# Kernel tuning notes

Measured on AMD Instinct MI355X. Metric: run time of the kernel, lower is better.

Reference implementation:

```python
import jax, jax.numpy as jnp
import numpy as np

NUM_ENTITY = 500000
NUM_RELATION = 6000
NUM_WORD = 200000
D = 100          # entity_dim == word_dim
L = 3            # num_layer
B, E, F, Q = 16, 2000, 8000, 20
PAGERANK_LAMBDA = 0.8
FACT_SCALE = 3.0
VERY_NEG = -1e11
VERY_SMALL = 1e-10


def setup_inputs() -> dict:
    key = jax.random.key(0)
    ks = jax.random.split(key, 24)
    s = 0.05
    return {
        'local_entity': jax.random.randint(ks[0], (B, E), 0, NUM_ENTITY),
        'kb_fact_rel': jax.random.randint(ks[1], (B, F), 0, NUM_RELATION),
        'kb_head': jax.random.randint(ks[2], (B, F), 0, E),
        'kb_tail': jax.random.randint(ks[3], (B, F), 0, E),
        'query_text': jax.random.randint(ks[4], (B, Q), 0, NUM_WORD),
        'q2e_adj_mat': jax.random.uniform(ks[5], (B, E, 1)),
        'entity_table': jax.random.normal(ks[6], (NUM_ENTITY + 1, D)) * s,
        'rel_table': jax.random.normal(ks[7], (NUM_RELATION + 1, D)) * s,
        'word_table': jax.random.normal(ks[8], (NUM_WORD + 1, D)) * s,
        'rel_lin_w': jax.random.normal(ks[9], (D, D)) * s,
        'rel_lin_b': jnp.zeros((D,)),
        'lstm_wih': jax.random.normal(ks[10], (4 * D, D)) * s,
        'lstm_whh': jax.random.normal(ks[11], (4 * D, D)) * s,
        'lstm_bih': jnp.zeros((4 * D,)),
        'lstm_bhh': jnp.zeros((4 * D,)),
        'q2e_w': jax.random.normal(ks[12], (L, D, D)) * s,
        'q2e_b': jnp.zeros((L, D)),
        'e2q_w': jax.random.normal(ks[13], (L, D, 3 * D)) * s,
        'e2q_b': jnp.zeros((L, D)),
        'e2e_w': jax.random.normal(ks[14], (L, D, 3 * D)) * s,
        'e2e_b': jnp.zeros((L, D)),
        'head_w': jax.random.normal(ks[15], (L, D, D)) * s,
        'head_b': jnp.zeros((L, D)),
        'tail_w': jax.random.normal(ks[16], (L, D, D)) * s,
        'tail_b': jnp.zeros((L, D)),
        'self_w': jax.random.normal(ks[17], (L, D, D)) * s,
        'self_b': jnp.zeros((L, D)),
        'score_w': jax.random.normal(ks[18], (1, D)) * s,
        'score_b': jnp.zeros((1,)),
    }


def _lstm(x, wih, whh, bih, bhh):
    # x: (B, Q, D); torch LSTM gate order i,f,g,o
    b = x.shape[0]
    h0 = jnp.zeros((b, D), x.dtype)

    def step(carry, xt):
        h, c = carry
        g = xt @ wih.T + h @ whh.T + bih + bhh
        i, f, gg, o = jnp.split(g, 4, axis=-1)
        c = jax.nn.sigmoid(f) * c + jax.nn.sigmoid(i) * jnp.tanh(gg)
        h = jax.nn.sigmoid(o) * jnp.tanh(c)
        return (h, c), h

    (h, _), hs = jax.lax.scan(step, (h0, h0), x.transpose(1, 0, 2))
    return hs.transpose(1, 0, 2), h


def _gather(x, idx):
    # sparse_bmm(entity2fact, x): out[b,f] = x[b, head[b,f]]
    return jnp.take_along_axis(x, idx[:, :, None], axis=1)


def _scatter(x, idx, num):
    # sparse_bmm(fact2entity, x): segment-sum facts onto tail entities
    b, f, d = x.shape
    flat = (idx + jnp.arange(b)[:, None] * num).reshape(-1)
    return jax.ops.segment_sum(x.reshape(b * f, d), flat, num_segments=b * num).reshape(b, num, d)


def reference(local_entity, kb_fact_rel, kb_head, kb_tail, query_text, q2e_adj_mat,
              entity_table, rel_table, word_table, rel_lin_w, rel_lin_b,
              lstm_wih, lstm_whh, lstm_bih, lstm_bhh,
              q2e_w, q2e_b, e2q_w, e2q_b, e2e_w, e2e_b,
              head_w, head_b, tail_w, tail_b, self_w, self_b, score_w, score_b):
    div = float(np.sqrt(D))
    q_mask = (query_text != NUM_WORD).astype(jnp.float32)
    e_mask = (local_entity != NUM_ENTITY).astype(jnp.float32)

    # query LSTM encoding
    q_emb = word_table[query_text]                                   # (B,Q,D)
    q_hidden, q_last = _lstm(q_emb, lstm_wih, lstm_whh, lstm_bih, lstm_bhh)
    query_node_emb = q_last[:, None, :]                              # (B,1,D)

    # fact embeddings from relations
    fact_emb = rel_table[kb_fact_rel] @ rel_lin_w.T + rel_lin_b      # (B,F,D)

    # fact-to-query attention weights (softmax over query words)
    sim = jnp.einsum('bqd,bfd->bqf', q_hidden, fact_emb) / div
    sim = jax.nn.softmax(sim + (1.0 - q_mask)[:, :, None] * VERY_NEG, axis=1)
    att = jnp.einsum('bqf,bqd->bfd', sim, q_hidden)                  # (B,F,D)
    Wf = jnp.sum(att * fact_emb, axis=2) / div                       # (B,F)
    W_tilde = jnp.exp(Wf - Wf.max(axis=1, keepdims=True))
    e2f_softmax = jnp.clip(_scatter(W_tilde[:, :, None], kb_head, E)[:, :, 0], VERY_SMALL, None)

    local_entity_emb = entity_table[local_entity]                    # (B,E,D)
    pagerank_f = q2e_adj_mat[:, :, 0]                                # (B,E)

    for i in range(L):
        q2e_emb = jnp.broadcast_to(query_node_emb @ q2e_w[i].T + q2e_b[i], (B, E, D))
        # entity -> fact (gather heads)
        e2f = jax.nn.relu(fact_emb @ self_w[i].T + self_b[i] +
                          _gather(local_entity_emb @ head_w[i].T + head_b[i], kb_head))
        e2f = e2f * (W_tilde[:, :, None] * _gather((pagerank_f / e2f_softmax)[:, :, None], kb_head))
        # fact -> entity (scatter to tails)
        f2e = jax.nn.relu(local_entity_emb @ self_w[i].T + self_b[i] +
                          FACT_SCALE * _scatter(e2f @ tail_w[i].T + tail_b[i], kb_tail, E))
        # pagerank propagation
        pr = _scatter(_gather(pagerank_f[:, :, None], kb_head), kb_tail, E)[:, :, 0]
        pagerank_f = PAGERANK_LAMBDA * pr + (1.0 - PAGERANK_LAMBDA) * pagerank_f
        # k=3 concat -> e2q / e2e updates
        nxt = jnp.concatenate([local_entity_emb, q2e_emb, f2e], axis=2)   # (B,E,3D)
        query_node_emb = jnp.einsum('be,bed->bd', pagerank_f, nxt @ e2q_w[i].T + e2q_b[i])[:, None, :]
        local_entity_emb = jax.nn.relu(nxt @ e2e_w[i].T + e2e_b[i])

    score = (local_entity_emb @ score_w.T + score_b)[:, :, 0]
    return score + (1.0 - e_mask) * VERY_NEG
```

## Files before the change

### kernel.cpp

```cpp
#include <hip/hip_runtime.h>
#include <math.h>

namespace {

typedef unsigned short u16;
typedef short bf16x8 __attribute__((ext_vector_type(8)));
typedef float f32x4 __attribute__((ext_vector_type(4)));

constexpr int B = 16, E = 2000, F = 8000, Q = 20, D = 100, NLAYER = 3;
constexpr int NUM_ENTITY_C = 500000;
constexpr int NREL1 = 6001;
constexpr int SK = 128;
constexpr int WFSZ = 28 * 64 * 8;
constexpr float PAGERANK_LAMBDA = 0.8f;
constexpr float FACT_SCALE = 3.0f;
constexpr float VERY_NEG = -100000000000.0f;
constexpr float VERY_SMALL = 1e-10f;

__device__ __forceinline__ float sigf(float x) { return 1.0f / (1.0f + __expf(-x)); }

__device__ __forceinline__ short f2bf(float f) {
    union { float f; unsigned int u; } c; c.f = f;
    unsigned int u = c.u + 0x7FFF + ((c.u >> 16) & 1);
    return (short)(u >> 16);
}
__device__ __forceinline__ float bf2f(u16 s) {
    union { unsigned int u; float f; } c; c.u = ((unsigned int)s) << 16;
    return c.f;
}

__global__ void wprep_kernel(const float* __restrict__ rel_lin_w,
                             const float* __restrict__ self_w, const float* __restrict__ head_w,
                             const float* __restrict__ tail_w, const float* __restrict__ e2e_w,
                             u16* __restrict__ WF)
{
    int m = blockIdx.y;
    int ns = blockIdx.x;
    int n = ns >> 2, s = ns & 3;
    int lane = threadIdx.x;
    const float* W; int ldW = D, kofs = 0; float scale = 1.f;
    if (m == 0) { W = rel_lin_w; }
    else {
        int L = (m - 1) / 5, t = (m - 1) % 5;
        if (t == 0)      { W = self_w + (size_t)L * D * D; }
        else if (t == 1) { W = head_w + (size_t)L * D * D; }
        else if (t == 2) { W = tail_w + (size_t)L * D * D; scale = FACT_SCALE; }
        else if (t == 3) { W = e2e_w + (size_t)L * D * 3 * D; ldW = 3 * D; }
        else             { W = e2e_w + (size_t)L * D * 3 * D; ldW = 3 * D; kofs = 2 * D; }
    }
    int col = n * 16 + (lane & 15);
    int kb = s * 32 + (lane >> 4) * 8;
    bf16x8 f;
#pragma unroll
    for (int j = 0; j < 8; ++j) {
        int k = kb + j;
        float v = (col < D && k < D) ? scale * W[(size_t)col * ldW + kofs + k] : 0.f;
        f[j] = f2bf(v);
    }
    *reinterpret_cast<bf16x8*>(WF + ((size_t)m * 28 + ns) * 64 * 8 + lane * 8) = f;
}

__global__ void qhprep_kernel(const float* __restrict__ qh, u16* __restrict__ qhB)
{
    int b = blockIdx.x;
    int t = threadIdx.x;
    int ns = t >> 6;
    int lane = t & 63;
    int n = ns >> 2, s = ns & 3;
    int q = n * 16 + (lane & 15);
    int kb = s * 32 + (lane >> 4) * 8;
    bf16x8 f;
#pragma unroll
    for (int j = 0; j < 8; ++j) {
        int k = kb + j;
        float v = (q < Q && k < D) ? qh[((size_t)b * Q + q) * D + k] : 0.f;
        f[j] = f2bf(v);
    }
    *reinterpret_cast<bf16x8*>(qhB + ((size_t)(b * 8 + ns) * 64 + lane) * 8) = f;
}

__global__ __launch_bounds__(256, 2) void wfm_kernel(const u16* __restrict__ REL,
                                                     const int* __restrict__ frel,
                                                     const u16* __restrict__ qhB,
                                                     float* __restrict__ wt, int nrows)
{
    const int lane = threadIdx.x & 63;
    const int lrow = lane & 15, lkg = lane >> 4;
    const int wv = blockIdx.x * (blockDim.x >> 6) + (threadIdx.x >> 6);
    const int nwv = gridDim.x * (blockDim.x >> 6);
    const int nch = nrows >> 4;

    for (int chunk = wv; chunk < nch; chunk += nwv) {
        const int row = chunk * 16 + lrow;
        const int b = (chunk * 16) / F;
        bf16x8 af[4];
        {
            const u16* src = REL + (size_t)frel[row] * SK;
#pragma unroll
            for (int s = 0; s < 4; ++s)
                af[s] = *reinterpret_cast<const bf16x8*>(src + s * 32 + lkg * 8);
        }
        f32x4 acc[2];
        acc[0] = (f32x4){0.f, 0.f, 0.f, 0.f};
        acc[1] = (f32x4){0.f, 0.f, 0.f, 0.f};
#pragma unroll
        for (int s = 0; s < 4; ++s) {
#pragma unroll
            for (int n = 0; n < 2; ++n) {
                bf16x8 qb = *reinterpret_cast<const bf16x8*>(
                    qhB + ((size_t)(b * 8 + n * 4 + s) * 64 + lane) * 8);
                acc[n] = __builtin_amdgcn_mfma_f32_16x16x32_bf16(af[s], qb, acc[n], 0, 0, 0);
            }
        }
        const bool v1 = lrow < (Q - 16);
#pragma unroll
        for (int r = 0; r < 4; ++r) {
            float s0 = acc[0][r] * 0.1f;
            float s1 = acc[1][r] * 0.1f;
            float m = v1 ? fmaxf(s0, s1) : s0;
#pragma unroll
            for (int d = 1; d < 16; d <<= 1) m = fmaxf(m, __shfl_xor(m, d));
            float e0 = __expf(s0 - m);
            float e1 = v1 ? __expf(s1 - m) : 0.f;
            float sum = e0 + e1;
            float wsum = fmaf(e0, s0, e1 * s1);
#pragma unroll
            for (int d = 1; d < 16; d <<= 1) {
                sum += __shfl_xor(sum, d);
                wsum += __shfl_xor(wsum, d);
            }
            if (lrow == 0) wt[chunk * 16 + lkg * 4 + r] = wsum / sum;
        }
    }
}

template<int A1S, int A2S, int EPI, bool OUTBF>
__global__ __launch_bounds__(256, 2) void mm2(
    const void* __restrict__ A1p, const int* __restrict__ idx1, int lda1,
    const void* __restrict__ A2p, const int* __restrict__ idx2,
    const u16* __restrict__ WF1, const u16* __restrict__ WF2,
    const float* __restrict__ b1, const float* __restrict__ b2,
    const float* __restrict__ vq,
    const float* __restrict__ wtv, const float* __restrict__ prv,
    const int* __restrict__ row_start,
    const float* __restrict__ prOld, const int* __restrict__ sheadv,
    float* __restrict__ prNew,
    void* __restrict__ outp, int nrows)
{
    const int lane = threadIdx.x & 63;
    const int lrow = lane & 15, lkg = lane >> 4;
    const int wv = blockIdx.x * (blockDim.x >> 6) + (threadIdx.x >> 6);
    const int nwv = gridDim.x * (blockDim.x >> 6);
    const int nch = (nrows + 15) >> 4;

    bf16x8 w1[7][4];
#pragma unroll
    for (int n = 0; n < 7; ++n)
#pragma unroll
        for (int s = 0; s < 4; ++s)
            w1[n][s] = *reinterpret_cast<const bf16x8*>(WF1 + ((size_t)(n * 4 + s) * 64 + lane) * 8);

    for (int chunk = wv; chunk < nch; chunk += nwv) {
        const int row = chunk * 16 + lrow;
        const int ar = row < nrows ? row : nrows - 1;

        bf16x8 af1[4];
        if (A1S == 0) {
            const u16* src = (const u16*)A1p + (size_t)ar * SK;
#pragma unroll
            for (int s = 0; s < 4; ++s)
                af1[s] = *reinterpret_cast<const bf16x8*>(src + s * 32 + lkg * 8);
        } else if (A1S == 1) {
            const u16* src = (const u16*)A1p + (size_t)idx1[ar] * SK;
#pragma unroll
            for (int s = 0; s < 4; ++s)
                af1[s] = *reinterpret_cast<const bf16x8*>(src + s * 32 + lkg * 8);
        } else {
            const float* arow = (const float*)A1p + (size_t)ar * lda1;
#pragma unroll
            for (int s = 0; s < 4; ++s) {
                const int k0 = s * 32 + lkg * 8;
                float tv[8];
                if (k0 + 8 <= D) {
                    float4 v0 = *reinterpret_cast<const float4*>(arow + k0);
                    float4 v1 = *reinterpret_cast<const float4*>(arow + k0 + 4);
                    tv[0]=v0.x; tv[1]=v0.y; tv[2]=v0.z; tv[3]=v0.w;
                    tv[4]=v1.x; tv[5]=v1.y; tv[6]=v1.z; tv[7]=v1.w;
                } else {
#pragma unroll
                    for (int j = 0; j < 8; ++j) tv[j] = (k0 + j < D) ? arow[k0 + j] : 0.f;
                }
                bf16x8 f;
#pragma unroll
                for (int j = 0; j < 8; ++j) f[j] = f2bf(tv[j]);
                af1[s] = f;
            }
        }

        int s0 = 0, s1 = 0;
        if (A2S == 2) { s0 = row_start[ar]; s1 = row_start[ar + 1]; }

        bf16x8 af2[4];
        if (A2S == 1) {
            const u16* src = (const u16*)A2p + (size_t)idx2[ar] * SK;
#pragma unroll
            for (int s = 0; s < 4; ++s)
                af2[s] = *reinterpret_cast<const bf16x8*>(src + s * 32 + lkg * 8);
        } else if (A2S == 3) {
            const u16* src = (const u16*)A2p + (size_t)ar * SK;
#pragma unroll
            for (int s = 0; s < 4; ++s)
                af2[s] = *reinterpret_cast<const bf16x8*>(src + s * 32 + lkg * 8);
        }

        f32x4 acc[7];
#pragma unroll
        for (int n = 0; n < 7; ++n) acc[n] = (f32x4){0.f, 0.f, 0.f, 0.f};
#pragma unroll
        for (int s = 0; s < 4; ++s) {
#pragma unroll
            for (int n = 0; n < 7; ++n)
                acc[n] = __builtin_amdgcn_mfma_f32_16x16x32_bf16(af1[s], w1[n][s], acc[n], 0, 0, 0);
            if (A2S == 1 || A2S == 3) {
#pragma unroll
                for (int n = 0; n < 7; ++n) {
                    bf16x8 w2 = *reinterpret_cast<const bf16x8*>(
                        WF2 + ((size_t)(n * 4 + s) * 64 + lane) * 8);
                    acc[n] = __builtin_amdgcn_mfma_f32_16x16x32_bf16(af2[s], w2, acc[n], 0, 0, 0);
                }
            } else if (A2S == 2) {
                float a2f[8];
#pragma unroll
                for (int j = 0; j < 8; ++j) a2f[j] = 0.f;
                for (int i = s0; i < s1; ++i) {
                    bf16x8 v = *reinterpret_cast<const bf16x8*>(
                        (const u16*)A2p + (size_t)i * SK + s * 32 + lkg * 8);
#pragma unroll
                    for (int j = 0; j < 8; ++j) a2f[j] += bf2f((u16)v[j]);
                }
                bf16x8 fsum;
#pragma unroll
                for (int j = 0; j < 8; ++j) fsum[j] = f2bf(a2f[j]);
#pragma unroll
                for (int n = 0; n < 7; ++n) {
                    bf16x8 w2 = *reinterpret_cast<const bf16x8*>(
                        WF2 + ((size_t)(n * 4 + s) * 64 + lane) * 8);
                    acc[n] = __builtin_amdgcn_mfma_f32_16x16x32_bf16(fsum, w2, acc[n], 0, 0, 0);
                }
            }
        }
        if (A2S == 2 && lkg == 0 && row < nrows) {
            float a = 0.f;
            for (int i = s0; i < s1; ++i) a += prOld[sheadv[i]];
            prNew[row] = PAGERANK_LAMBDA * a + (1.0f - PAGERANK_LAMBDA) * prOld[row];
        }

        const int rb = chunk * 16 + lkg * 4;
#pragma unroll
        for (int r = 0; r < 4; ++r) {
            const int orow = rb + r;
            if (orow >= nrows) continue;
            float rsv = 1.f, cntf = 0.f; int vb = 0;
            if (EPI == 1) rsv = wtv[orow] * prv[idx2[orow]];
            if (EPI == 2) cntf = (float)(row_start[orow + 1] - row_start[orow]);
            if (EPI == 3) vb = orow / E;
#pragma unroll
            for (int n = 0; n < 7; ++n) {
                const int col = n * 16 + lrow;
                if (col >= D) continue;
                float v = acc[n][r];
                if (b1) v += b1[col];
                if (EPI == 1) v += b2[col];
                if (EPI == 2) v += FACT_SCALE * cntf * b2[col];
                if (EPI == 3) v += vq[vb * D + col];
                if (EPI != 0) v = fmaxf(v, 0.f);
                if (EPI == 1) v *= rsv;
                if (OUTBF) ((u16*)outp)[(size_t)orow * SK + col] = (u16)f2bf(v);
                else       ((float*)outp)[(size_t)orow * D + col] = v;
            }
        }
    }
}

__global__ __launch_bounds__(512) void gatesx_kernel(
    const int* __restrict__ qtext, const float* __restrict__ wtab,
    const float* __restrict__ wih, const float* __restrict__ bih,
    const float* __restrict__ bhh, float* __restrict__ gx)
{
    int row = blockIdx.x;
    int t = threadIdx.x;
    __shared__ __align__(16) float xs[D];
    if (t < D) xs[t] = wtab[(size_t)qtext[row] * D + t];
    __syncthreads();
    if (t < 4 * D) {
        const float4* w4 = reinterpret_cast<const float4*>(wih + (size_t)t * D);
        const float4* x4 = reinterpret_cast<const float4*>(xs);
        float a0 = 0.f, a1 = 0.f, a2 = 0.f, a3 = 0.f;
#pragma unroll
        for (int k = 0; k < 25; ++k) {
            float4 wv = w4[k]; float4 xv = x4[k];
            a0 = fmaf(wv.x, xv.x, a0); a1 = fmaf(wv.y, xv.y, a1);
            a2 = fmaf(wv.z, xv.z, a2); a3 = fmaf(wv.w, xv.w, a3);
        }
        gx[(size_t)row * (4 * D) + t] = a0 + a1 + a2 + a3 + bih[t] + bhh[t];
    }
}

__global__ __launch_bounds__(512) void lstmrec_kernel(
    const float* __restrict__ gx, const float* __restrict__ whh,
    float* __restrict__ q_hidden, float* __restrict__ qne)
{
    int b = blockIdx.x, t = threadIdx.x;
    __shared__ __align__(16) float h[D];
    __shared__ float cst[D];
    __shared__ float g[4 * D];
    float4 w[25];
    if (t < 4 * D) {
        const float4* wr = reinterpret_cast<const float4*>(whh + (size_t)t * D);
#pragma unroll
        for (int k = 0; k < 25; ++k) w[k] = wr[k];
    }
    if (t < D) { h[t] = 0.f; cst[t] = 0.f; }
    __syncthreads();
    for (int step = 0; step < Q; ++step) {
        if (t < 4 * D) {
            const float4* h4 = reinterpret_cast<const float4*>(h);
            float a0 = 0.f, a1 = 0.f, a2 = 0.f, a3 = 0.f;
#pragma unroll
            for (int k = 0; k < 25; ++k) {
                float4 hv = h4[k];
                a0 = fmaf(w[k].x, hv.x, a0); a1 = fmaf(w[k].y, hv.y, a1);
                a2 = fmaf(w[k].z, hv.z, a2); a3 = fmaf(w[k].w, hv.w, a3);
            }
            g[t] = a0 + a1 + a2 + a3 + gx[((size_t)b * Q + step) * (4 * D) + t];
        }
        __syncthreads();
        if (t < D) {
            float gi = g[t], gf = g[t + D], gg = g[t + 2 * D], go = g[t + 3 * D];
            float cn = sigf(gf) * cst[t] + sigf(gi) * tanhf(gg);
            float hn = sigf(go) * tanhf(cn);
            cst[t] = cn; h[t] = hn;
            q_hidden[((size_t)b * Q + step) * D + t] = hn;
            if (step == Q - 1) qne[b * D + t] = hn;
        }
        __syncthreads();
    }
}

__global__ void idxabs_kernel(const int* __restrict__ kb_head, const int* __restrict__ kb_tail,
                              int* __restrict__ headAbs, int* __restrict__ tailAbs,
                              int* __restrict__ counts)
{
    int r = blockIdx.x * 256 + threadIdx.x;
    if (r < B * F) {
        int b = r / F;
        headAbs[r] = b * E + kb_head[r];
        int t = b * E + kb_tail[r];
        tailAbs[r] = t;
        atomicAdd(&counts[t], 1);
    }
}

__global__ __launch_bounds__(1024) void scan_kernel(const int* __restrict__ counts,
                                                    int* __restrict__ row_start,
                                                    int* __restrict__ cursor)
{
    __shared__ int part[1024];
    int t = threadIdx.x;
    int base = t * 32;
    int local[32];
    int s = 0;
#pragma unroll
    for (int i = 0; i < 32; ++i) {
        int idx = base + i;
        int v = (idx < B * E) ? counts[idx] : 0;
        local[i] = s; s += v;
    }
    part[t] = s;
    __syncthreads();
    for (int off = 1; off < 1024; off <<= 1) {
        int v = (t >= off) ? part[t - off] : 0;
        __syncthreads();
        if (t >= off) part[t] += v;
        __syncthreads();
    }
    int prev = (t > 0) ? part[t - 1] : 0;
#pragma unroll
    for (int i = 0; i < 32; ++i) {
        int idx = base + i;
        if (idx < B * E) { int rs = prev + local[i]; row_start[idx] = rs; cursor[idx] = rs; }
    }
    if (t == 1023) row_start[B * E] = part[1023];
}

__global__ void fill_kernel(const int* __restrict__ tailAbs, int* __restrict__ cursor,
                            int* __restrict__ factlist)
{
    int r = blockIdx.x * 256 + threadIdx.x;
    if (r < B * F) {
        int p = atomicAdd(&cursor[tailAbs[r]], 1);
        factlist[p] = r;
    }
}

__global__ void sprep_kernel(const int* __restrict__ factlist, const int* __restrict__ frel,
                             const int* __restrict__ headAbs, const float* __restrict__ wt,
                             const float* __restrict__ e2fsm,
                             int* __restrict__ srel, int* __restrict__ shead,
                             float* __restrict__ srsv)
{
    int i = blockIdx.x * 256 + threadIdx.x;
    if (i < B * F) {
        int fl = factlist[i];
        int h = headAbs[fl];
        srel[i] = frel[fl];
        shead[i] = h;
        srsv[i] = wt[fl] / fmaxf(e2fsm[h], VERY_SMALL);
    }
}

__global__ void rowmax_kernel(const float* __restrict__ Wf, float* __restrict__ Wmax)
{
    int b = blockIdx.x, tid = threadIdx.x;
    float m = -3.4e38f;
    for (int i = tid; i < F; i += 256) m = fmaxf(m, Wf[(size_t)b * F + i]);
#pragma unroll
    for (int o = 32; o > 0; o >>= 1) m = fmaxf(m, __shfl_down(m, o));
    __shared__ float sm[4];
    if ((tid & 63) == 0) sm[tid >> 6] = m;
    __syncthreads();
    if (tid == 0) Wmax[b] = fmaxf(fmaxf(sm[0], sm[1]), fmaxf(sm[2], sm[3]));
}

__global__ void wtilde_kernel(float* __restrict__ wt, const float* __restrict__ Wmax,
                              const int* __restrict__ headAbs, float* __restrict__ e2fsm)
{
    int r = blockIdx.x * 256 + threadIdx.x;
    if (r < B * F) {
        int b = r / F;
        float v = __expf(wt[r] - Wmax[b]);
        wt[r] = v;
        atomicAdd(&e2fsm[headAbs[r]], v);
    }
}

__global__ void entgather_kernel(const int* __restrict__ local_entity,
                                 const float* __restrict__ etab, u16* __restrict__ emb,
                                 const float* __restrict__ q2e_adj, float* __restrict__ pr)
{
    int i = blockIdx.x * 256 + threadIdx.x;
    if (i < B * E) pr[i] = q2e_adj[i];
    if (i < B * E * 25) {
        int row = i / 25, p = i - row * 25;
        float4 v = reinterpret_cast<const float4*>(etab + (size_t)local_entity[row] * D)[p];
        short4 o;
        o.x = f2bf(v.x); o.y = f2bf(v.y); o.z = f2bf(v.z); o.w = f2bf(v.w);
        *reinterpret_cast<short4*>(emb + (size_t)row * SK + p * 4) = o;
    }
}

__global__ void qvec_kernel(const float* __restrict__ qne, const float* __restrict__ q2ew,
                            const float* __restrict__ q2eb, const float* __restrict__ e2ew,
                            float* __restrict__ q2e_vec, float* __restrict__ vq)
{
    int b = blockIdx.x, t = threadIdx.x;
    __shared__ float qv[D];
    __shared__ float qn[D];
    if (t < D) qn[t] = qne[b * D + t];
    __syncthreads();
    if (t < D) {
        const float* wr = q2ew + (size_t)t * D;
        float acc = q2eb[t];
        for (int k = 0; k < D; ++k) acc = fmaf(qn[k], wr[k], acc);
        qv[t] = acc; q2e_vec[b * D + t] = acc;
    }
    __syncthreads();
    if (t < D) {
        const float* wr = e2ew + (size_t)t * 300 + 100;
        float acc = 0.f;
        for (int k = 0; k < D; ++k) acc = fmaf(qv[k], wr[k], acc);
        vq[b * D + t] = acc;
    }
}

__global__ __launch_bounds__(256) void zsum_kernel(const float* __restrict__ pr,
                                                   const u16* __restrict__ emb,
                                                   const u16* __restrict__ f2e,
                                                   float* __restrict__ zpart)
{
    const int b = blockIdx.x, ch = blockIdx.y;
    const int t = threadIdx.x;
    const int g = t >> 4, tg = t & 15;
    const int ebase = ch * (E / 16);
    const int eend = ebase + (E / 16);
    float accA[8], accB[8];
#pragma unroll
    for (int j = 0; j < 8; ++j) { accA[j] = 0.f; accB[j] = 0.f; }
    float accp = 0.f;
    for (int e = ebase + g; e < eend; e += 16) {
        const float p = pr[b * E + e];
        const size_t ro = ((size_t)b * E + e) * SK + tg * 8;
        bf16x8 va = *reinterpret_cast<const bf16x8*>(emb + ro);
        bf16x8 vb = *reinterpret_cast<const bf16x8*>(f2e + ro);
#pragma unroll
        for (int j = 0; j < 8; ++j) {
            accA[j] = fmaf(p, bf2f((u16)va[j]), accA[j]);
            accB[j] = fmaf(p, bf2f((u16)vb[j]), accB[j]);
        }
        if (tg == 0) accp += p;
    }
    __shared__ float smA[16][132];
    __shared__ float smB[16][132];
    __shared__ float smp[16];
#pragma unroll
    for (int j = 0; j < 8; ++j) {
        smA[g][tg * 8 + j] = accA[j];
        smB[g][tg * 8 + j] = accB[j];
    }
    if (tg == 0) smp[g] = accp;
    __syncthreads();
    float* zp = zpart + (size_t)(b * 16 + ch) * 208;
    if (t < D) {
        float sa = 0.f, sb = 0.f;
#pragma unroll
        for (int gg = 0; gg < 16; ++gg) { sa += smA[gg][t]; sb += smB[gg][t]; }
        zp[t] = sa;
        zp[D + t] = sb;
    }
    if (t == 255) {
        float sp = 0.f;
#pragma unroll
        for (int gg = 0; gg < 16; ++gg) sp += smp[gg];
        zp[2 * D] = sp;
    }
}

__global__ void qne_kernel(const float* __restrict__ zpart, const float* __restrict__ q2ev,
                           const float* __restrict__ W, const float* __restrict__ bias,
                           float* __restrict__ qne)
{
    int b = blockIdx.x, t = threadIdx.x;
    __shared__ float zb[201];
    for (int i = t; i < 201; i += 128) {
        float s = 0.f;
        for (int ch = 0; ch < 16; ++ch) s += zpart[(size_t)(b * 16 + ch) * 208 + i];
        zb[i] = s;
    }
    __syncthreads();
    if (t >= D) return;
    float ps = zb[2 * D];
    const float* wr = W + (size_t)t * 3 * D;
    float acc = ps * bias[t];
    for (int k = 0; k < D; ++k) {
        acc = fmaf(zb[k], wr[k], acc);
        acc = fmaf(ps * q2ev[b * D + k], wr[D + k], acc);
        acc = fmaf(zb[D + k], wr[2 * D + k], acc);
    }
    qne[b * D + t] = acc;
}

__global__ __launch_bounds__(256) void score_kernel(const u16* __restrict__ emb,
                                                    const float* __restrict__ sw,
                                                    const float* __restrict__ sb,
                                                    const int* __restrict__ le,
                                                    float* __restrict__ outp)
{
    __shared__ float rows[64 * 106];
    __shared__ float sws[D];
    int r0 = blockIdx.x * 64, tid = threadIdx.x;
    for (int i = tid; i < 64 * 16; i += 256) {
        int r = i >> 4, c = i & 15;
        if (c < 13) {
            bf16x8 raw = *reinterpret_cast<const bf16x8*>(emb + (size_t)(r0 + r) * SK + c * 8);
#pragma unroll
            for (int j = 0; j < 8; ++j) rows[r * 106 + c * 8 + j] = bf2f((u16)raw[j]);
        }
    }
    if (tid < D) sws[tid] = sw[tid];
    __syncthreads();
    if (tid < 64) {
        float acc = sb[0];
        const float* rr = &rows[tid * 106];
        for (int k = 0; k < D; ++k) acc = fmaf(rr[k], sws[k], acc);
        int r = r0 + tid;
        outp[r] = acc + ((le[r] != NUM_ENTITY_C) ? 0.0f : VERY_NEG);
    }
}

int mmgrid(int nrows) {
    int ch = (nrows + 15) / 16;
    int blocks = (ch + 3) / 4;
    return blocks < 512 ? blocks : 512;
}

}

extern "C" void kernel_launch(void* const* d_in, const int* in_sizes, int n_in,
                              void* d_out, int out_size, void* d_ws, size_t ws_size,
                              hipStream_t stream)
{
    (void)in_sizes; (void)n_in; (void)out_size;
    const int*   local_entity = (const int*)d_in[0];
    const int*   kb_fact_rel  = (const int*)d_in[1];
    const int*   kb_head      = (const int*)d_in[2];
    const int*   kb_tail      = (const int*)d_in[3];
    const int*   query_text   = (const int*)d_in[4];
    const float* q2e_adj      = (const float*)d_in[5];
    const float* entity_table = (const float*)d_in[6];
    const float* rel_table    = (const float*)d_in[7];
    const float* word_table   = (const float*)d_in[8];
    const float* rel_lin_w    = (const float*)d_in[9];
    const float* rel_lin_b    = (const float*)d_in[10];
    const float* lstm_wih     = (const float*)d_in[11];
    const float* lstm_whh     = (const float*)d_in[12];
    const float* lstm_bih     = (const float*)d_in[13];
    const float* lstm_bhh     = (const float*)d_in[14];
    const float* q2e_w        = (const float*)d_in[15];
    const float* q2e_b        = (const float*)d_in[16];
    const float* e2q_w        = (const float*)d_in[17];
    const float* e2q_b        = (const float*)d_in[18];
    const float* e2e_w        = (const float*)d_in[19];
    const float* e2e_b        = (const float*)d_in[20];
    const float* head_w       = (const float*)d_in[21];
    const float* head_b       = (const float*)d_in[22];
    const float* tail_w       = (const float*)d_in[23];
    const float* tail_b       = (const float*)d_in[24];
    const float* self_w       = (const float*)d_in[25];
    const float* self_b       = (const float*)d_in[26];
    const float* score_w      = (const float*)d_in[27];
    const float* score_b      = (const float*)d_in[28];
    float* out = (float*)d_out;

    float* ws = (float*)d_ws;
    size_t o = 0;
    auto alloc = [&](size_t n) { float* p = ws + o; o += (n + 3) & ~(size_t)3; return p; };
    float* q_hidden = alloc((size_t)B * Q * D);
    float* qne      = alloc(B * D);
    float* gx       = alloc((size_t)B * Q * 4 * D);
    float* wt       = alloc((size_t)B * F);
    float* wmax     = alloc(16);
    float* e2fsm    = alloc(B * E);
    int*   counts   = (int*)alloc(B * E);
    float* pr0      = alloc(B * E);
    float* pr1      = alloc(B * E);
    float* q2e_vec  = alloc(B * D);
    float* vq       = alloc(B * D);
    float* zpart    = alloc((size_t)B * 16 * 208);
    float* srsv     = alloc((size_t)B * F);
    u16* WF   = (u16*)alloc((size_t)16 * WFSZ / 2);
    u16* qhB  = (u16*)alloc((size_t)B * 8 * 64 * 8 / 2);
    u16* REL  = (u16*)alloc((size_t)NREL1 * SK / 2 + 64);
    u16* emb0 = (u16*)alloc((size_t)B * E * SK / 2);
    u16* emb1 = (u16*)alloc((size_t)B * E * SK / 2);
    u16* e2fS = (u16*)alloc((size_t)B * F * SK / 2);
    u16* f2e  = (u16*)alloc((size_t)B * E * SK / 2);
    int* headAbs  = (int*)alloc((size_t)B * F);
    int* tailAbs  = (int*)alloc((size_t)B * F);
    int* row_start= (int*)alloc(B * E + 1);
    int* cursor   = (int*)alloc(B * E);
    int* factlist = (int*)alloc((size_t)B * F);
    int* srel     = (int*)alloc((size_t)B * F);
    int* shead    = (int*)alloc((size_t)B * F);
    if (ws_size < o * sizeof(float)) return;

    auto WFm = [&](int m) { return WF + (size_t)m * WFSZ; };

    wprep_kernel<<<dim3(28, 16), dim3(64), 0, stream>>>(rel_lin_w, self_w, head_w, tail_w,
                                                        e2e_w, WF);
    gatesx_kernel<<<dim3(B * Q), dim3(512), 0, stream>>>(query_text, word_table, lstm_wih,
                                                         lstm_bih, lstm_bhh, gx);
    lstmrec_kernel<<<dim3(B), dim3(512), 0, stream>>>(gx, lstm_whh, q_hidden, qne);
    qhprep_kernel<<<dim3(B), dim3(512), 0, stream>>>(q_hidden, qhB);
    hipMemsetAsync(e2fsm, 0, (size_t)2 * B * E * sizeof(float), stream);
    idxabs_kernel<<<dim3((B * F + 255) / 256), dim3(256), 0, stream>>>(
        kb_head, kb_tail, headAbs, tailAbs, counts);
    scan_kernel<<<dim3(1), dim3(1024), 0, stream>>>(counts, row_start, cursor);
    fill_kernel<<<dim3((B * F + 255) / 256), dim3(256), 0, stream>>>(tailAbs, cursor, factlist);

    mm2<2, 0, 0, true><<<dim3(mmgrid(NREL1)), dim3(256), 0, stream>>>(
        rel_table, nullptr, D, nullptr, nullptr, WFm(0), nullptr, rel_lin_b, nullptr,
        nullptr, nullptr, nullptr, nullptr, nullptr, nullptr, nullptr,
        REL, NREL1);

    wfm_kernel<<<dim3(mmgrid(B * F)), dim3(256), 0, stream>>>(REL, kb_fact_rel, qhB, wt, B * F);
    rowmax_kernel<<<dim3(B), dim3(256), 0, stream>>>(wt, wmax);
    wtilde_kernel<<<dim3((B * F + 255) / 256), dim3(256), 0, stream>>>(wt, wmax, headAbs, e2fsm);
    sprep_kernel<<<dim3((B * F + 255) / 256), dim3(256), 0, stream>>>(
        factlist, kb_fact_rel, headAbs, wt, e2fsm, srel, shead, srsv);
    entgather_kernel<<<dim3((B * E * 25 + 255) / 256), dim3(256), 0, stream>>>(
        local_entity, entity_table, emb0, q2e_adj, pr0);

    u16* embO = emb0; u16* embN = emb1;
    float* prO = pr0; float* prN = pr1;
    for (int i = 0; i < NLAYER; ++i) {
        const float* q2e_wi  = q2e_w + (size_t)i * D * D;
        const float* q2e_bi  = q2e_b + i * D;
        const float* e2q_wi  = e2q_w + (size_t)i * D * 3 * D;
        const float* e2q_bi  = e2q_b + i * D;
        const float* e2e_wi  = e2e_w + (size_t)i * D * 3 * D;
        const float* e2e_bi  = e2e_b + i * D;
        const float* head_bi = head_b + i * D;
        const float* tail_bi = tail_b + i * D;
        const float* self_bi = self_b + i * D;
        const u16* wf_self = WFm(1 + i * 5 + 0);
        const u16* wf_head = WFm(1 + i * 5 + 1);
        const u16* wf_tail = WFm(1 + i * 5 + 2);
        const u16* wf_e2e0 = WFm(1 + i * 5 + 3);
        const u16* wf_e2e2 = WFm(1 + i * 5 + 4);

        qvec_kernel<<<dim3(B), dim3(128), 0, stream>>>(qne, q2e_wi, q2e_bi, e2e_wi,
                                                       q2e_vec, vq);
        mm2<1, 1, 1, true><<<dim3(mmgrid(B * F)), dim3(256), 0, stream>>>(
            REL, srel, 0, embO, shead, wf_self, wf_head, self_bi, head_bi,
            nullptr, srsv, prO, nullptr, nullptr, nullptr, nullptr,
            e2fS, B * F);
        mm2<0, 2, 2, true><<<dim3(mmgrid(B * E)), dim3(256), 0, stream>>>(
            embO, nullptr, 0, e2fS, nullptr, wf_self, wf_tail, self_bi, tail_bi,
            nullptr, nullptr, nullptr, row_start, prO, shead, prN,
            f2e, B * E);
        zsum_kernel<<<dim3(B, 16), dim3(256), 0, stream>>>(prN, embO, f2e, zpart);
        qne_kernel<<<dim3(B), dim3(128), 0, stream>>>(zpart, q2e_vec, e2q_wi, e2q_bi, qne);
        mm2<0, 3, 3, true><<<dim3(mmgrid(B * E)), dim3(256), 0, stream>>>(
            embO, nullptr, 0, f2e, nullptr, wf_e2e0, wf_e2e2, e2e_bi, nullptr,
            vq, nullptr, nullptr, nullptr, nullptr, nullptr, nullptr,
            embN, B * E);
        { u16* tmp = embO; embO = embN; embN = tmp; }
        { float* tmp = prO; prO = prN; prN = tmp; }
    }
    score_kernel<<<dim3((B * E) / 64), dim3(256), 0, stream>>>(
        embO, score_w, score_b, local_entity, out);
}
```

Measured before the change: 624.3 us.

## Fuse softmax, zsum, qne, score and fact-sort steps into neighbouring kernels

Folds the exp and head-sum atomics into wfm_kernel and drops the per-batch row-max pass; the max shift cancels in the W_tilde ratio. Merges fill and sprep into one scatter kernel. Moves the pagerank-weighted z reduction into the f2e mm2 epilogue via atomics, and the e2q/qne product into the next layer's qvec kernel. Folds the score projection into the last e2e mm2 and skips pagerank/z work in the final layer. This removes several launches and a re-read of emb/f2e, at the cost of more global atomics, dropping the max shift inside exp, and a grid change for the entity-side mm2s.

Measured after the change: 738.5 us. 18.3% more time.

```diff
diff --git a/kernel.cpp b/kernel.cpp
--- a/kernel.cpp
+++ b/kernel.cpp
@@ -82,7 +82,9 @@
 __global__ __launch_bounds__(256, 2) void wfm_kernel(const u16* __restrict__ REL,
                                                      const int* __restrict__ frel,
                                                      const u16* __restrict__ qhB,
-                                                     float* __restrict__ wt, int nrows)
+                                                     const int* __restrict__ headAbs,
+                                                     float* __restrict__ wt,
+                                                     float* __restrict__ e2fsm, int nrows)
 {
     const int lane = threadIdx.x & 63;
     const int lrow = lane & 15, lkg = lane >> 4;
@@ -129,12 +131,17 @@
                 sum += __shfl_xor(sum, d);
                 wsum += __shfl_xor(wsum, d);
             }
-            if (lrow == 0) wt[chunk * 16 + lkg * 4 + r] = wsum / sum;
-        }
-    }
-}
-
-template<int A1S, int A2S, int EPI, bool OUTBF>
+            if (lrow == 0) {
+                int orow = chunk * 16 + lkg * 4 + r;
+                float wtl = __expf(wsum / sum);
+                wt[orow] = wtl;
+                atomicAdd(&e2fsm[headAbs[orow]], wtl);
+            }
+        }
+    }
+}
+
+template<int A1S, int A2S, int EPI, bool OUTBF, bool PRZ>
 __global__ __launch_bounds__(256, 2) void mm2(
     const void* __restrict__ A1p, const int* __restrict__ idx1, int lda1,
     const void* __restrict__ A2p, const int* __restrict__ idx2,
@@ -144,7 +151,7 @@
     const float* __restrict__ wtv, const float* __restrict__ prv,
     const int* __restrict__ row_start,
     const float* __restrict__ prOld, const int* __restrict__ sheadv,
-    float* __restrict__ prNew,
+    float* __restrict__ prNew, float* __restrict__ zacc,
     void* __restrict__ outp, int nrows)
 {
     const int lane = threadIdx.x & 63;
@@ -249,21 +256,34 @@
                 }
             }
         }
-        if (A2S == 2 && lkg == 0 && row < nrows) {
-            float a = 0.f;
-            for (int i = s0; i < s1; ++i) a += prOld[sheadv[i]];
-            prNew[row] = PAGERANK_LAMBDA * a + (1.0f - PAGERANK_LAMBDA) * prOld[row];
+        float prn = 0.f;
+        if (PRZ) {
+            if (lkg == 0) {
+                float a = 0.f;
+                for (int i = s0; i < s1; ++i) a += prOld[sheadv[i]];
+                prn = PAGERANK_LAMBDA * a + (1.0f - PAGERANK_LAMBDA) * prOld[row];
+                prNew[row] = prn;
+            }
         }
 
         const int rb = chunk * 16 + lkg * 4;
+        const int bb = (chunk * 16) / E;
+        float prr[4];
+        float zf[7];
+        if (PRZ) {
+#pragma unroll
+            for (int r = 0; r < 4; ++r) prr[r] = __shfl(prn, lkg * 4 + r);
+#pragma unroll
+            for (int n = 0; n < 7; ++n) zf[n] = 0.f;
+        }
 #pragma unroll
         for (int r = 0; r < 4; ++r) {
             const int orow = rb + r;
             if (orow >= nrows) continue;
-            float rsv = 1.f, cntf = 0.f; int vb = 0;
+            float rsv = 1.f, cntf = 0.f;
             if (EPI == 1) rsv = wtv[orow] * prv[idx2[orow]];
             if (EPI == 2) cntf = (float)(row_start[orow + 1] - row_start[orow]);
-            if (EPI == 3) vb = orow / E;
+            float scr = 0.f;
 #pragma unroll
             for (int n = 0; n < 7; ++n) {
                 const int col = n * 16 + lrow;
@@ -272,12 +292,60 @@
                 if (b1) v += b1[col];
                 if (EPI == 1) v += b2[col];
                 if (EPI == 2) v += FACT_SCALE * cntf * b2[col];
-                if (EPI == 3) v += vq[vb * D + col];
+                if (EPI == 3 || EPI == 4) v += vq[bb * D + col];
                 if (EPI != 0) v = fmaxf(v, 0.f);
                 if (EPI == 1) v *= rsv;
-                if (OUTBF) ((u16*)outp)[(size_t)orow * SK + col] = (u16)f2bf(v);
-                else       ((float*)outp)[(size_t)orow * D + col] = v;
-            }
+                if (PRZ) zf[n] += prr[r] * v;
+                if (EPI == 4) {
+                    scr = fmaf(v, b2[col], scr);
+                } else {
+                    if (OUTBF) ((u16*)outp)[(size_t)orow * SK + col] = (u16)f2bf(v);
+                    else       ((float*)outp)[(size_t)orow * D + col] = v;
+                }
+            }
+            if (EPI == 4) {
+                scr += __shfl_xor(scr, 1);
+                scr += __shfl_xor(scr, 2);
+                scr += __shfl_xor(scr, 4);
+                scr += __shfl_xor(scr, 8);
+                if (lrow == 0) {
+                    float s = scr + prOld[0] +
+                              ((sheadv[orow] != NUM_ENTITY_C) ? 0.f : VERY_NEG);
+                    ((float*)outp)[orow] = s;
+                }
+            }
+        }
+        if (PRZ) {
+            float* zb = zacc + bb * 201;
+#pragma unroll
+            for (int n = 0; n < 7; ++n) {
+                float t0 = zf[n];
+                t0 += __shfl_xor(t0, 16);
+                t0 += __shfl_xor(t0, 32);
+                if (lkg == 0) {
+                    int col = n * 16 + lrow;
+                    if (col < D) atomicAdd(&zb[D + col], t0);
+                }
+            }
+            float w = __shfl(prn, lrow);
+#pragma unroll
+            for (int s = 0; s < 4; ++s)
+#pragma unroll
+                for (int j = 0; j < 8; ++j) {
+                    float t0 = w * bf2f((u16)af1[s][j]);
+                    t0 += __shfl_xor(t0, 1);
+                    t0 += __shfl_xor(t0, 2);
+                    t0 += __shfl_xor(t0, 4);
+                    t0 += __shfl_xor(t0, 8);
+                    int k = s * 32 + lkg * 8 + j;
+                    if (lrow == 0 && k < D) atomicAdd(&zb[k], t0);
+                }
+            float t0 = (lkg == 0) ? prn : 0.f;
+            t0 += __shfl_xor(t0, 1);
+            t0 += __shfl_xor(t0, 2);
+            t0 += __shfl_xor(t0, 4);
+            t0 += __shfl_xor(t0, 8);
+            if (lane == 0) atomicAdd(&zb[2 * D], t0);
         }
     }
 }
@@ -393,54 +461,19 @@
     if (t == 1023) row_start[B * E] = part[1023];
 }
 
-__global__ void fill_kernel(const int* __restrict__ tailAbs, int* __restrict__ cursor,
-                            int* __restrict__ factlist)
+__global__ void fillsprep_kernel(const int* __restrict__ tailAbs, int* __restrict__ cursor,
+                                 const int* __restrict__ headAbs, const int* __restrict__ frel,
+                                 const float* __restrict__ wt, const float* __restrict__ e2fsm,
+                                 int* __restrict__ srel, int* __restrict__ shead,
+                                 float* __restrict__ srsv)
 {
     int r = blockIdx.x * 256 + threadIdx.x;
     if (r < B * F) {
         int p = atomicAdd(&cursor[tailAbs[r]], 1);
-        factlist[p] = r;
-    }
-}
-
-__global__ void sprep_kernel(const int* __restrict__ factlist, const int* __restrict__ frel,
-                             const int* __restrict__ headAbs, const float* __restrict__ wt,
-                             const float* __restrict__ e2fsm,
-                             int* __restrict__ srel, int* __restrict__ shead,
-                             float* __restrict__ srsv)
-{
-    int i = blockIdx.x * 256 + threadIdx.x;
-    if (i < B * F) {
-        int fl = factlist[i];
-        int h = headAbs[fl];
-        srel[i] = frel[fl];
-        shead[i] = h;
-        srsv[i] = wt[fl] / fmaxf(e2fsm[h], VERY_SMALL);
-    }
-}
-
-__global__ void rowmax_kernel(const float* __restrict__ Wf, float* __restrict__ Wmax)
-{
-    int b = blockIdx.x, tid = threadIdx.x;
-    float m = -3.4e38f;
-    for (int i = tid; i < F; i += 256) m = fmaxf(m, Wf[(size_t)b * F + i]);
-#pragma unroll
-    for (int o = 32; o > 0; o >>= 1) m = fmaxf(m, __shfl_down(m, o));
-    __shared__ float sm[4];
-    if ((tid & 63) == 0) sm[tid >> 6] = m;
-    __syncthreads();
-    if (tid == 0) Wmax[b] = fmaxf(fmaxf(sm[0], sm[1]), fmaxf(sm[2], sm[3]));
-}
-
-__global__ void wtilde_kernel(float* __restrict__ wt, const float* __restrict__ Wmax,
-                              const int* __restrict__ headAbs, float* __restrict__ e2fsm)
-{
-    int r = blockIdx.x * 256 + threadIdx.x;
-    if (r < B * F) {
-        int b = r / F;
-        float v = __expf(wt[r] - Wmax[b]);
-        wt[r] = v;
-        atomicAdd(&e2fsm[headAbs[r]], v);
+        int h = headAbs[r];
+        srel[p] = frel[r];
+        shead[p] = h;
+        srsv[p] = wt[r] / fmaxf(e2fsm[h], VERY_SMALL);
     }
 }
 
@@ -459,23 +492,46 @@
     }
 }
 
-__global__ void qvec_kernel(const float* __restrict__ qne, const float* __restrict__ q2ew,
-                            const float* __restrict__ q2eb, const float* __restrict__ e2ew,
+template<bool HASQNE>
+__global__ void qvec_kernel(const float* __restrict__ qneIn, float* __restrict__ z,
+                            const float* __restrict__ e2qw, const float* __restrict__ e2qb,
+                            const float* __restrict__ q2ew, const float* __restrict__ q2eb,
+                            const float* __restrict__ e2ew,
                             float* __restrict__ q2e_vec, float* __restrict__ vq)
 {
     int b = blockIdx.x, t = threadIdx.x;
+    __shared__ float qn[D];
     __shared__ float qv[D];
-    __shared__ float qn[D];
-    if (t < D) qn[t] = qne[b * D + t];
+    __shared__ float zb[201];
+    float* zg = z + b * 201;
+    if (HASQNE) {
+        for (int i = t; i < 201; i += 128) { zb[i] = zg[i]; zg[i] = 0.f; }
+        __syncthreads();
+        if (t < D) {
+            float ps = zb[2 * D];
+            const float* wr = e2qw + (size_t)t * 3 * D;
+            float acc = ps * e2qb[t];
+            for (int k = 0; k < D; ++k) {
+                acc = fmaf(zb[k], wr[k], acc);
+                acc = fmaf(ps * q2e_vec[b * D + k], wr[D + k], acc);
+                acc = fmaf(zb[D + k], wr[2 * D + k], acc);
+            }
+            qn[t] = acc;
+        }
+    } else {
+        for (int i = t; i < 201; i += 128) zg[i] = 0.f;
+        if (t < D) qn[t] = qneIn[b * D + t];
+    }
     __syncthreads();
     if (t < D) {
         const float* wr = q2ew + (size_t)t * D;
         float acc = q2eb[t];
         for (int k = 0; k < D; ++k) acc = fmaf(qn[k], wr[k], acc);
-        qv[t] = acc; q2e_vec[b * D + t] = acc;
+        qv[t] = acc;
     }
     __syncthreads();
     if (t < D) {
+        q2e_vec[b * D + t] = qv[t];
         const float* wr = e2ew + (size_t)t * 300 + 100;
         float acc = 0.f;
         for (int k = 0; k < D; ++k) acc = fmaf(qv[k], wr[k], acc);
@@ -483,113 +539,14 @@
     }
 }
 
-__global__ __launch_bounds__(256) void zsum_kernel(const float* __restrict__ pr,
-                                                   const u16* __restrict__ emb,
-                                                   const u16* __restrict__ f2e,
-                                                   float* __restrict__ zpart)
-{
-    const int b = blockIdx.x, ch = blockIdx.y;
-    const int t = threadIdx.x;
-    const int g = t >> 4, tg = t & 15;
-    const int ebase = ch * (E / 16);
-    const int eend = ebase + (E / 16);
-    float accA[8], accB[8];
-#pragma unroll
-    for (int j = 0; j < 8; ++j) { accA[j] = 0.f; accB[j] = 0.f; }
-    float accp = 0.f;
-    for (int e = ebase + g; e < eend; e += 16) {
-        const float p = pr[b * E + e];
-        const size_t ro = ((size_t)b * E + e) * SK + tg * 8;
-        bf16x8 va = *reinterpret_cast<const bf16x8*>(emb + ro);
-        bf16x8 vb = *reinterpret_cast<const bf16x8*>(f2e + ro);
-#pragma unroll
-        for (int j = 0; j < 8; ++j) {
-            accA[j] = fmaf(p, bf2f((u16)va[j]), accA[j]);
-            accB[j] = fmaf(p, bf2f((u16)vb[j]), accB[j]);
-        }
-        if (tg == 0) accp += p;
-    }
-    __shared__ float smA[16][132];
-    __shared__ float smB[16][132];
-    __shared__ float smp[16];
-#pragma unroll
-    for (int j = 0; j < 8; ++j) {
-        smA[g][tg * 8 + j] = accA[j];
-        smB[g][tg * 8 + j] = accB[j];
-    }
-    if (tg == 0) smp[g] = accp;
-    __syncthreads();
-    float* zp = zpart + (size_t)(b * 16 + ch) * 208;
-    if (t < D) {
-        float sa = 0.f, sb = 0.f;
-#pragma unroll
-        for (int gg = 0; gg < 16; ++gg) { sa += smA[gg][t]; sb += smB[gg][t]; }
-        zp[t] = sa;
-        zp[D + t] = sb;
-    }
-    if (t == 255) {
-        float sp = 0.f;
-#pragma unroll
-        for (int gg = 0; gg < 16; ++gg) sp += smp[gg];
-        zp[2 * D] = sp;
-    }
-}
-
-__global__ void qne_kernel(const float* __restrict__ zpart, const float* __restrict__ q2ev,
-                           const float* __restrict__ W, const float* __restrict__ bias,
-                           float* __restrict__ qne)
-{
-    int b = blockIdx.x, t = threadIdx.x;
-    __shared__ float zb[201];
-    for (int i = t; i < 201; i += 128) {
-        float s = 0.f;
-        for (int ch = 0; ch < 16; ++ch) s += zpart[(size_t)(b * 16 + ch) * 208 + i];
-        zb[i] = s;
-    }
-    __syncthreads();
-    if (t >= D) return;
-    float ps = zb[2 * D];
-    const float* wr = W + (size_t)t * 3 * D;
-    float acc = ps * bias[t];
-    for (int k = 0; k < D; ++k) {
-        acc = fmaf(zb[k], wr[k], acc);
-        acc = fmaf(ps * q2ev[b * D + k], wr[D + k], acc);
-        acc = fmaf(zb[D + k], wr[2 * D + k], acc);
-    }
-    qne[b * D + t] = acc;
-}
-
-__global__ __launch_bounds__(256) void score_kernel(const u16* __restrict__ emb,
-                                                    const float* __restrict__ sw,
-                                                    const float* __restrict__ sb,
-                                                    const int* __restrict__ le,
-                                                    float* __restrict__ outp)
-{
-    __shared__ float rows[64 * 106];
-    __shared__ float sws[D];
-    int r0 = blockIdx.x * 64, tid = threadIdx.x;
-    for (int i = tid; i < 64 * 16; i += 256) {
-        int r = i >> 4, c = i & 15;
-        if (c < 13) {
-            bf16x8 raw = *reinterpret_cast<const bf16x8*>(emb + (size_t)(r0 + r) * SK + c * 8);
-#pragma unroll
-            for (int j = 0; j < 8; ++j) rows[r * 106 + c * 8 + j] = bf2f((u16)raw[j]);
-        }
-    }
-    if (tid < D) sws[tid] = sw[tid];
-    __syncthreads();
-    if (tid < 64) {
-        float acc = sb[0];
-        const float* rr = &rows[tid * 106];
-        for (int k = 0; k < D; ++k) acc = fmaf(rr[k], sws[k], acc);
-        int r = r0 + tid;
-        outp[r] = acc + ((le[r] != NUM_ENTITY_C) ? 0.0f : VERY_NEG);
-    }
-}
-
 int mmgrid(int nrows) {
     int ch = (nrows + 15) / 16;
     int blocks = (ch + 3) / 4;
+    return blocks < 512 ? blocks : 512;
+}
+int mmgrid8(int nrows) {
+    int ch = (nrows + 15) / 16;
+    int blocks = (ch + 7) / 8;
     return blocks < 512 ? blocks : 512;
 }
 
@@ -638,14 +595,13 @@
     float* qne      = alloc(B * D);
     float* gx       = alloc((size_t)B * Q * 4 * D);
     float* wt       = alloc((size_t)B * F);
-    float* wmax     = alloc(16);
     float* e2fsm    = alloc(B * E);
     int*   counts   = (int*)alloc(B * E);
     float* pr0      = alloc(B * E);
     float* pr1      = alloc(B * E);
     float* q2e_vec  = alloc(B * D);
     float* vq       = alloc(B * D);
-    float* zpart    = alloc((size_t)B * 16 * 208);
+    float* z        = alloc(B * 201);
     float* srsv     = alloc((size_t)B * F);
     u16* WF   = (u16*)alloc((size_t)16 * WFSZ / 2);
     u16* qhB  = (u16*)alloc((size_t)B * 8 * 64 * 8 / 2);
@@ -658,7 +614,6 @@
     int* tailAbs  = (int*)alloc((size_t)B * F);
     int* row_start= (int*)alloc(B * E + 1);
     int* cursor   = (int*)alloc(B * E);
-    int* factlist = (int*)alloc((size_t)B * F);
     int* srel     = (int*)alloc((size_t)B * F);
     int* shead    = (int*)alloc((size_t)B * F);
     if (ws_size < o * sizeof(float)) return;
@@ -675,18 +630,14 @@
     idxabs_kernel<<<dim3((B * F + 255) / 256), dim3(256), 0, stream>>>(
         kb_head, kb_tail, headAbs, tailAbs, counts);
     scan_kernel<<<dim3(1), dim3(1024), 0, stream>>>(counts, row_start, cursor);
-    fill_kernel<<<dim3((B * F + 255) / 256), dim3(256), 0, stream>>>(tailAbs, cursor, factlist);
-
-    mm2<2, 0, 0, true><<<dim3(mmgrid(NREL1)), dim3(256), 0, stream>>>(
+    mm2<2, 0, 0, true, false><<<dim3(mmgrid(NREL1)), dim3(256), 0, stream>>>(
         rel_table, nullptr, D, nullptr, nullptr, WFm(0), nullptr, rel_lin_b, nullptr,
-        nullptr, nullptr, nullptr, nullptr, nullptr, nullptr, nullptr,
+        nullptr, nullptr, nullptr, nullptr, nullptr, nullptr, nullptr, nullptr,
         REL, NREL1);
-
-    wfm_kernel<<<dim3(mmgrid(B * F)), dim3(256), 0, stream>>>(REL, kb_fact_rel, qhB, wt, B * F);
-    rowmax_kernel<<<dim3(B), dim3(256), 0, stream>>>(wt, wmax);
-    wtilde_kernel<<<dim3((B * F + 255) / 256), dim3(256), 0, stream>>>(wt, wmax, headAbs, e2fsm);
-    sprep_kernel<<<dim3((B * F + 255) / 256), dim3(256), 0, stream>>>(
-        factlist, kb_fact_rel, headAbs, wt, e2fsm, srel, shead, srsv);
+    wfm_kernel<<<dim3(mmgrid(B * F)), dim3(256), 0, stream>>>(
+        REL, kb_fact_rel, qhB, headAbs, wt, e2fsm, B * F);
+    fillsprep_kernel<<<dim3((B * F + 255) / 256), dim3(256), 0, stream>>>(
+        tailAbs, cursor, headAbs, kb_fact_rel, wt, e2fsm, srel, shead, srsv);
     entgather_kernel<<<dim3((B * E * 25 + 255) / 256), dim3(256), 0, stream>>>(
         local_entity, entity_table, emb0, q2e_adj, pr0);
 
@@ -695,8 +646,6 @@
     for (int i = 0; i < NLAYER; ++i) {
         const float* q2e_wi  = q2e_w + (size_t)i * D * D;
         const float* q2e_bi  = q2e_b + i * D;
-        const float* e2q_wi  = e2q_w + (size_t)i * D * 3 * D;
-        const float* e2q_bi  = e2q_b + i * D;
         const float* e2e_wi  = e2e_w + (size_t)i * D * 3 * D;
         const float* e2e_bi  = e2e_b + i * D;
         const float* head_bi = head_b + i * D;
@@ -707,26 +656,41 @@
         const u16* wf_tail = WFm(1 + i * 5 + 2);
         const u16* wf_e2e0 = WFm(1 + i * 5 + 3);
         const u16* wf_e2e2 = WFm(1 + i * 5 + 4);
-
-        qvec_kernel<<<dim3(B), dim3(128), 0, stream>>>(qne, q2e_wi, q2e_bi, e2e_wi,
-                                                       q2e_vec, vq);
-        mm2<1, 1, 1, true><<<dim3(mmgrid(B * F)), dim3(256), 0, stream>>>(
+        const bool last = (i == NLAYER - 1);
+
+        if (i == 0)
+            qvec_kernel<false><<<dim3(B), dim3(128), 0, stream>>>(
+                qne, z, nullptr, nullptr, q2e_wi, q2e_bi, e2e_wi, q2e_vec, vq);
+        else
+            qvec_kernel<true><<<dim3(B), dim3(128), 0, stream>>>(
+                nullptr, z, e2q_w + (size_t)(i - 1) * D * 3 * D, e2q_b + (size_t)(i - 1) * D,
+                q2e_wi, q2e_bi, e2e_wi, q2e_vec, vq);
+
+        mm2<1, 1, 1, true, false><<<dim3(mmgrid(B * F)), dim3(256), 0, stream>>>(
             REL, srel, 0, embO, shead, wf_self, wf_head, self_bi, head_bi,
-            nullptr, srsv, prO, nullptr, nullptr, nullptr, nullptr,
+            nullptr, srsv, prO, nullptr, nullptr, nullptr, nullptr, nullptr,
             e2fS, B * F);
-        mm2<0, 2, 2, true><<<dim3(mmgrid(B * E)), dim3(256), 0, stream>>>(
-            embO, nullptr, 0, e2fS, nullptr, wf_self, wf_tail, self_bi, tail_bi,
-            nullptr, nullptr, nullptr, row_start, prO, shead, prN,
-            f2e, B * E);
-        zsum_kernel<<<dim3(B, 16), dim3(256), 0, stream>>>(prN, embO, f2e, zpart);
-        qne_kernel<<<dim3(B), dim3(128), 0, stream>>>(zpart, q2e_vec, e2q_wi, e2q_bi, qne);
-        mm2<0, 3, 3, true><<<dim3(mmgrid(B * E)), dim3(256), 0, stream>>>(
-            embO, nullptr, 0, f2e, nullptr, wf_e2e0, wf_e2e2, e2e_bi, nullptr,
-            vq, nullptr, nullptr, nullptr, nullptr, nullptr, nullptr,
-            embN, B * E);
+        if (!last)
+            mm2<0, 2, 2, true, true><<<dim3(mmgrid8(B * E)), dim3(256), 0, stream>>>(
+                embO, nullptr, 0, e2fS, nullptr, wf_self, wf_tail, self_bi, tail_bi,
+                nullptr, nullptr, nullptr, row_start, prO, shead, prN, z,
+                f2e, B * E);
+        else
+            mm2<0, 2, 2, true, false><<<dim3(mmgrid8(B * E)), dim3(256), 0, stream>>>(
+                embO, nullptr, 0, e2fS, nullptr, wf_self, wf_tail, self_bi, tail_bi,
+                nullptr, nullptr, nullptr, row_start, nullptr, nullptr, nullptr, nullptr,
+                f2e, B * E);
+        if (!last)
+            mm2<0, 3, 3, true, false><<<dim3(mmgrid8(B * E)), dim3(256), 0, stream>>>(
+                embO, nullptr, 0, f2e, nullptr, wf_e2e0, wf_e2e2, e2e_bi, nullptr,
+                vq, nullptr, nullptr, nullptr, nullptr, nullptr, nullptr, nullptr,
+                embN, B * E);
+        else
+            mm2<0, 3, 4, false, false><<<dim3(mmgrid8(B * E)), dim3(256), 0, stream>>>(
+                embO, nullptr, 0, f2e, nullptr, wf_e2e0, wf_e2e2, e2e_bi, score_w,
+                vq, nullptr, nullptr, nullptr, score_b, local_entity, nullptr, nullptr,
+                out, B * E);
         { u16* tmp = embO; embO = embN; embN = tmp; }
         { float* tmp = prO; prO = prN; prN = tmp; }
     }
-    score_kernel<<<dim3((B * E) / 64), dim3(256), 0, stream>>>(
-        embO, score_w, score_b, local_entity, out);
-}
+}
```
